# Kernel optimization log

Measured on AMD Instinct MI355X. Metric: run time of the kernel, lower is better.

## Reference

```python
import jax, jax.numpy as jnp
import numpy as np

B, T, E, H = 64, 200, 512, 8
D = E // H          # head size 64
SCALE = E ** -0.5   # NOTE: original scales by EMBED_DIM**-0.5, not head_size**-0.5


def _ln(x, g, b):
    mu = jnp.mean(x, axis=-1, keepdims=True)
    d = x - mu
    v = jnp.mean(d * d, axis=-1, keepdims=True)
    return g * d * jax.lax.rsqrt(v + 1e-5) + b


def _forward(idx, memory, src_mask, pred_mask,
             sa_wq, sa_wk, sa_wv, sa_wo, sa_bo,
             ca_wq, ca_wk, ca_wv, ca_wo, ca_bo,
             f_w1, f_b1, f_w2, f_b2,
             ln1_g, ln1_b, ln2_g, ln2_b, ln3_g, ln3_b):
    causal = jnp.tril(jnp.ones((T, T), dtype=bool))      # [T,T]
    pm = (pred_mask != 0)[:, None, :, None]              # [B,1,T,1]
    sm = (src_mask != 0)[:, None, :, None]               # [B,1,T,1]

    # --- masked multi-head self-attention (query AND key zeroed by pred_mask) ---
    h = _ln(idx, ln1_g, ln1_b)
    q = jnp.where(pm, jnp.einsum('bte,hed->bhtd', h, sa_wq), 0.0)
    k = jnp.where(pm, jnp.einsum('bte,hed->bhtd', h, sa_wk), 0.0)
    v = jnp.einsum('bte,hed->bhtd', h, sa_wv)
    s = jnp.einsum('bhtd,bhsd->bhts', q, k) * SCALE
    s = jnp.where(causal, s, -jnp.inf)
    w = jax.nn.softmax(s, axis=-1)
    o = jnp.einsum('bhts,bhsd->bthd', w, v).reshape(B, T, E)
    idx = o @ sa_wo + sa_bo + idx

    # --- cross-attention: keys from memory (src-masked), VALUES FROM x (per original code) ---
    h = _ln(idx, ln2_g, ln2_b)
    q = jnp.einsum('bte,hed->bhtd', h, ca_wq)
    k = jnp.where(sm, jnp.einsum('bse,hed->bhsd', memory, ca_wk), 0.0)
    v = jnp.einsum('bte,hed->bhtd', h, ca_wv)
    s = jnp.einsum('bhtd,bhsd->bhts', q, k) * SCALE
    s = jnp.where(causal, s, -jnp.inf)   # mask=True in Decoder's ca
    w = jax.nn.softmax(s, axis=-1)
    o = jnp.einsum('bhts,bhsd->bthd', w, v).reshape(B, T, E)
    idx = o @ ca_wo + ca_bo + idx

    # --- feed-forward ---
    h = _ln(idx, ln3_g, ln3_b)
    idx = jax.nn.relu(h @ f_w1 + f_b1) @ f_w2 + f_b2 + idx
    return idx


def setup_inputs() -> dict:
    key = jax.random.key(0)
    ks = jax.random.split(key, 20)
    nrm = lambda k, sh: jax.random.normal(k, sh, jnp.float32) * 0.02
    return {
        'idx': jax.random.normal(ks[0], (B, T, E), jnp.float32),
        'memory': jax.random.normal(ks[1], (B, T, E), jnp.float32),
        'src_mask': jax.random.randint(ks[2], (B, T), 0, 2, jnp.int32),
        'pred_mask': jax.random.randint(ks[3], (B, T), 0, 2, jnp.int32),
        'sa_wq': nrm(ks[4], (H, E, D)), 'sa_wk': nrm(ks[5], (H, E, D)),
        'sa_wv': nrm(ks[6], (H, E, D)),
        'sa_wo': nrm(ks[7], (E, E)), 'sa_bo': jnp.zeros((E,), jnp.float32),
        'ca_wq': nrm(ks[8], (H, E, D)), 'ca_wk': nrm(ks[9], (H, E, D)),
        'ca_wv': nrm(ks[10], (H, E, D)),
        'ca_wo': nrm(ks[11], (E, E)), 'ca_bo': jnp.zeros((E,), jnp.float32),
        'f_w1': nrm(ks[12], (E, 4 * E)), 'f_b1': jnp.zeros((4 * E,), jnp.float32),
        'f_w2': nrm(ks[13], (4 * E, E)), 'f_b2': jnp.zeros((E,), jnp.float32),
        'ln1_g': jnp.ones((E,), jnp.float32), 'ln1_b': jnp.zeros((E,), jnp.float32),
        'ln2_g': jnp.ones((E,), jnp.float32), 'ln2_b': jnp.zeros((E,), jnp.float32),
        'ln3_g': jnp.ones((E,), jnp.float32), 'ln3_b': jnp.zeros((E,), jnp.float32),
    }


def reference(idx, memory, src_mask, pred_mask,
              sa_wq, sa_wk, sa_wv, sa_wo, sa_bo,
              ca_wq, ca_wk, ca_wv, ca_wo, ca_bo,
              f_w1, f_b1, f_w2, f_b2,
              ln1_g, ln1_b, ln2_g, ln2_b, ln3_g, ln3_b):
    return _forward(idx, memory, src_mask, pred_mask,
                    sa_wq, sa_wk, sa_wv, sa_wo, sa_bo,
                    ca_wq, ca_wk, ca_wv, ca_wo, ca_bo,
                    f_w1, f_b1, f_w2, f_b2,
                    ln1_g, ln1_b, ln2_g, ln2_b, ln3_g, ln3_b)
```

## Files before the change

kernel.cpp:

```cpp
#include <hip/hip_runtime.h>
#include <hip/hip_bf16.h>

#define B_ 64
#define T_ 200
#define E_ 512
#define H_ 8
#define D_ 64

static constexpr float SCALE = 0.044194173824159216f;

typedef __attribute__((ext_vector_type(8))) short bf16x8;
typedef __attribute__((ext_vector_type(4))) float f32x4;

static __device__ inline short f2bf(float f) {
    __hip_bfloat16 h = __float2bfloat16(f);
    return *(short*)&h;
}

static __device__ __forceinline__ void gload16(const short* g, short* l) {
    __builtin_amdgcn_global_load_lds(
        (const __attribute__((address_space(1))) void*)g,
        (__attribute__((address_space(3))) void*)l, 16, 0, 0);
}

__global__ void conv_kernel(const float* __restrict__ in,
                            __hip_bfloat16* __restrict__ out, int n) {
    int i = blockIdx.x * blockDim.x + threadIdx.x;
    if (i < n) out[i] = __float2bfloat16(in[i]);
}

template <int MODE>
__global__ void wt_kernel(const float* __restrict__ in,
                          __hip_bfloat16* __restrict__ out, int N, int K) {
    int i = blockIdx.x * blockDim.x + threadIdx.x;
    if (i >= N * K) return;
    int n = i / K, k = i - n * K;
    float v;
    if (MODE == 0) {
        v = in[(size_t)k * N + n];
    } else {
        int h = n >> 6, d = n & 63;
        v = in[((size_t)h * K + k) * 64 + d];
    }
    out[i] = __float2bfloat16(v);
}

__global__ __launch_bounds__(256) void ln_kernel(const float* __restrict__ x,
                                                 const float* __restrict__ g,
                                                 const float* __restrict__ bta,
                                                 __hip_bfloat16* __restrict__ out) {
    __shared__ float red[4];
    int row = blockIdx.x;
    const float* xr = x + (size_t)row * E_;
    int tid = threadIdx.x;
    float v0 = xr[tid], v1 = xr[tid + 256];
    float s = v0 + v1;
    for (int off = 32; off; off >>= 1) s += __shfl_down(s, off, 64);
    if ((tid & 63) == 0) red[tid >> 6] = s;
    __syncthreads();
    float mu = (red[0] + red[1] + red[2] + red[3]) * (1.0f / E_);
    __syncthreads();
    float d0 = v0 - mu, d1 = v1 - mu;
    float sq = d0 * d0 + d1 * d1;
    for (int off = 32; off; off >>= 1) sq += __shfl_down(sq, off, 64);
    if ((tid & 63) == 0) red[tid >> 6] = sq;
    __syncthreads();
    float var = (red[0] + red[1] + red[2] + red[3]) * (1.0f / E_);
    float r = rsqrtf(var + 1e-5f);
    out[(size_t)row * E_ + tid] = __float2bfloat16(g[tid] * d0 * r + bta[tid]);
    out[(size_t)row * E_ + tid + 256] =
        __float2bfloat16(g[tid + 256] * d1 * r + bta[tid + 256]);
}

template <int MSK, int RELU, int OM, int RES, int BIAS>
__global__ __launch_bounds__(256) void mgemm_kernel(
    const short* __restrict__ A, const short* __restrict__ BT,
    const float* __restrict__ bias, const int* __restrict__ rmask,
    const float* __restrict__ resid, void* __restrict__ Cv,
    int M, int N, int K, size_t wstep) {
    __shared__ __align__(16) short As[128 * 32];
    __shared__ __align__(16) short Bs[128 * 32];
    int tid = threadIdx.x;
    int wave = tid >> 6, lane = tid & 63;
    int qq = lane >> 4, l15 = lane & 15;
    int m0 = blockIdx.y * 128, n0 = blockIdx.x * 128;
    int wm = (wave & 1) * 64, wn = (wave >> 1) * 64;

    int srow = lane >> 2;
    int scol = ((lane & 3) ^ (srow & 3)) * 8;
    const short* gA = A + (size_t)(m0 + wave * 32 + srow) * K + scol;
    const short* gB = BT + (size_t)(n0 + wave * 32 + srow) * K + scol;
    short* lA = &As[wave * 1024];
    short* lB = &Bs[wave * 1024];
    size_t rstep = (size_t)16 * K;

    int swz = (qq ^ (l15 & 3)) * 8;

    f32x4 acc[4][4] = {};

    for (int k0 = 0; k0 < K; k0 += 32) {
        gload16(gA + k0, lA);
        gload16(gA + k0 + rstep, lA + 512);
        gload16(gB + k0, lB);
        gload16(gB + k0 + rstep, lB + 512);
        __syncthreads();
        bf16x8 af[4], bfr[4];
        #pragma unroll
        for (int i = 0; i < 4; ++i)
            af[i] = *(bf16x8*)(&As[(wm + i * 16 + l15) * 32 + swz]);
        #pragma unroll
        for (int j = 0; j < 4; ++j)
            bfr[j] = *(bf16x8*)(&Bs[(wn + j * 16 + l15) * 32 + swz]);
        #pragma unroll
        for (int i = 0; i < 4; ++i)
            #pragma unroll
            for (int j = 0; j < 4; ++j)
                acc[i][j] = __builtin_amdgcn_mfma_f32_16x16x32_bf16(
                    af[i], bfr[j], acc[i][j], 0, 0, 0);
        __syncthreads();
    }

    #pragma unroll
    for (int i = 0; i < 4; ++i) {
        #pragma unroll
        for (int r = 0; r < 4; ++r) {
            int row = m0 + wm + i * 16 + qq * 4 + r;
            float mval = 1.0f;
            if (MSK) mval = (rmask[row] != 0) ? 1.0f : 0.0f;
            #pragma unroll
            for (int j = 0; j < 4; ++j) {
                int col = n0 + wn + j * 16 + l15;
                float val = acc[i][j][r];
                if (BIAS) val += bias[col];
                if (MSK == 1) val *= mval;
                if (MSK == 2) { if (col < 1024) val *= mval; }
                if (RELU) val = fmaxf(val, 0.0f);
                if (RES) val += resid[(size_t)row * N + col];
                if (OM == 0) {
                    ((float*)Cv)[(size_t)row * N + col] = val;
                } else if (OM == 1) {
                    int b_ = row / T_, t = row - b_ * T_;
                    int hh = col >> 6, d = col & 63;
                    ((__hip_bfloat16*)Cv)[(((size_t)b_ * H_ + hh) * T_ + t) * D_ + d] =
                        __float2bfloat16(val);
                } else if (OM == 3) {
                    int b_ = row / T_, t = row - b_ * T_;
                    int which = col >> 9, cc = col & 511;
                    int hh = cc >> 6, d = cc & 63;
                    ((__hip_bfloat16*)Cv)[(size_t)which * wstep +
                                          (((size_t)b_ * H_ + hh) * T_ + t) * D_ + d] =
                        __float2bfloat16(val);
                } else {
                    ((__hip_bfloat16*)Cv)[(size_t)row * N + col] =
                        __float2bfloat16(val);
                }
            }
        }
    }
}

#define NQT 13
__global__ __launch_bounds__(256) void fattn_kernel(const short* __restrict__ q,
                                                    const short* __restrict__ k,
                                                    const short* __restrict__ v,
                                                    __hip_bfloat16* __restrict__ o) {
    __shared__ __align__(16) short Kf[NQT * 8 * 16 * 8];
    __shared__ __align__(16) short Vf[4 * 28 * 16 * 8];
    __shared__ __align__(16) short Pb[4 * 512];

    int tid = threadIdx.x;
    int wave = tid >> 6, lane = tid & 63;
    int qq = lane >> 4, l15 = lane & 15;
    int bh = blockIdx.x;
    int b = bh >> 3, h = bh & 7;

    const short* kp = k + (size_t)bh * T_ * D_;
    const short* vp = v + (size_t)bh * T_ * D_;
    const short* qp = q + (size_t)bh * T_ * D_;

    for (int idx = tid; idx < 8 * 208; idx += 256) {
        int g = idx / 208, s = idx - g * 208;
        int kt = s >> 4, l = s & 15;
        bf16x8 val;
        if (s < 200) {
            val = *(const bf16x8*)(kp + (size_t)s * 64 + g * 8);
        } else {
            #pragma unroll
            for (int j = 0; j < 8; ++j) val[j] = 0;
        }
        *(bf16x8*)&Kf[((kt * 8 + g) * 16 + l) * 8] = val;
    }
    for (int idx = tid; idx < 28 * 64; idx += 256) {
        int g = idx >> 6, d = idx & 63;
        int nt = d >> 4, dl = d & 15;
        bf16x8 val;
        if (g < 25) {
            #pragma unroll
            for (int j = 0; j < 8; ++j) val[j] = vp[(g * 8 + j) * 64 + d];
        } else {
            #pragma unroll
            for (int j = 0; j < 8; ++j) val[j] = 0;
        }
        *(bf16x8*)&Vf[((nt * 28 + g) * 16 + dl) * 8] = val;
    }
    __syncthreads();

    short* pb = &Pb[wave * 512];

    for (int qt = wave; qt < NQT; qt += 4) {
        int t0 = qt * 16;
        bf16x8 qf[2];
        #pragma unroll
        for (int ks = 0; ks < 2; ++ks)
            qf[ks] = *(const bf16x8*)(qp + (size_t)(t0 + l15) * 64 + ks * 32 + qq * 8);
        f32x4 sc[NQT];
        #pragma unroll
        for (int kt = 0; kt < NQT; ++kt) {
            f32x4 a = {0.f, 0.f, 0.f, 0.f};
            bf16x8 kf0 = *(const bf16x8*)&Kf[((kt * 8 + qq) * 16 + l15) * 8];
            bf16x8 kf1 = *(const bf16x8*)&Kf[((kt * 8 + 4 + qq) * 16 + l15) * 8];
            a = __builtin_amdgcn_mfma_f32_16x16x32_bf16(qf[0], kf0, a, 0, 0, 0);
            a = __builtin_amdgcn_mfma_f32_16x16x32_bf16(qf[1], kf1, a, 0, 0, 0);
            sc[kt] = a;
        }
        #pragma unroll
        for (int kt = 0; kt < NQT; ++kt) {
            #pragma unroll
            for (int r = 0; r < 4; ++r) {
                int col = kt * 16 + l15;
                int rowg = t0 + qq * 4 + r;
                sc[kt][r] = (col <= rowg) ? sc[kt][r] * SCALE : -1e30f;
            }
        }
        float mx[4], sum[4], inv[4];
        #pragma unroll
        for (int r = 0; r < 4; ++r) {
            float m = -1e30f;
            #pragma unroll
            for (int kt = 0; kt < NQT; ++kt) m = fmaxf(m, sc[kt][r]);
            #pragma unroll
            for (int off = 1; off < 16; off <<= 1)
                m = fmaxf(m, __shfl_xor(m, off, 64));
            mx[r] = m;
        }
        #pragma unroll
        for (int r = 0; r < 4; ++r) sum[r] = 0.f;
        #pragma unroll
        for (int kt = 0; kt < NQT; ++kt) {
            #pragma unroll
            for (int r = 0; r < 4; ++r) {
                float e = __expf(sc[kt][r] - mx[r]);
                sc[kt][r] = e;
                sum[r] += e;
            }
        }
        #pragma unroll
        for (int r = 0; r < 4; ++r) {
            float s = sum[r];
            #pragma unroll
            for (int off = 1; off < 16; off <<= 1) s += __shfl_xor(s, off, 64);
            inv[r] = 1.0f / s;
        }
        f32x4 oa[4] = {};
        #pragma unroll
        for (int c = 0; c < 7; ++c) {
            #pragma unroll
            for (int kt2 = 0; kt2 < 2; ++kt2) {
                int kt = c * 2 + kt2;
                int g = kt2 * 2 + (l15 >> 3);
                int jj = l15 & 7;
                #pragma unroll
                for (int r = 0; r < 4; ++r) {
                    float val = (kt < NQT) ? sc[kt][r] : 0.0f;
                    pb[(g * 16 + qq * 4 + r) * 8 + jj] = f2bf(val);
                }
            }
            bf16x8 pf = *(const bf16x8*)&pb[(qq * 16 + l15) * 8];
            #pragma unroll
            for (int nt = 0; nt < 4; ++nt) {
                bf16x8 vf = *(const bf16x8*)&Vf[((nt * 28 + c * 4 + qq) * 16 + l15) * 8];
                oa[nt] = __builtin_amdgcn_mfma_f32_16x16x32_bf16(pf, vf, oa[nt], 0, 0, 0);
            }
        }
        #pragma unroll
        for (int nt = 0; nt < 4; ++nt) {
            #pragma unroll
            for (int r = 0; r < 4; ++r) {
                int t = t0 + qq * 4 + r;
                if (t < T_) {
                    int d = nt * 16 + l15;
                    o[((size_t)b * T_ + t) * E_ + h * D_ + d] =
                        __float2bfloat16(oa[nt][r] * inv[r]);
                }
            }
        }
    }
}

extern "C" void kernel_launch(void* const* d_in, const int* in_sizes, int n_in,
                              void* d_out, int out_size, void* d_ws, size_t ws_size,
                              hipStream_t stream) {
    const float* idx    = (const float*)d_in[0];
    const float* memory = (const float*)d_in[1];
    const int* src_mask  = (const int*)d_in[2];
    const int* pred_mask = (const int*)d_in[3];
    const float* sa_wq = (const float*)d_in[4];
    const float* sa_wk = (const float*)d_in[5];
    const float* sa_wv = (const float*)d_in[6];
    const float* sa_wo = (const float*)d_in[7];
    const float* sa_bo = (const float*)d_in[8];
    const float* ca_wq = (const float*)d_in[9];
    const float* ca_wk = (const float*)d_in[10];
    const float* ca_wv = (const float*)d_in[11];
    const float* ca_wo = (const float*)d_in[12];
    const float* ca_bo = (const float*)d_in[13];
    const float* f_w1  = (const float*)d_in[14];
    const float* f_b1  = (const float*)d_in[15];
    const float* f_w2  = (const float*)d_in[16];
    const float* f_b2  = (const float*)d_in[17];
    const float* ln1_g = (const float*)d_in[18];
    const float* ln1_b = (const float*)d_in[19];
    const float* ln2_g = (const float*)d_in[20];
    const float* ln2_b = (const float*)d_in[21];
    const float* ln3_g = (const float*)d_in[22];
    const float* ln3_b = (const float*)d_in[23];
    float* out = (float*)d_out;

    const size_t BTE = (size_t)B_ * T_ * E_;
    const size_t EE = (size_t)E_ * E_;

    char* p = (char*)d_ws;
    short* qb = (short*)p;            p += BTE * 2;
    short* kb = (short*)p;            p += BTE * 2;
    short* vb = (short*)p;            p += BTE * 2;
    float* x1 = (float*)p;            p += BTE * 4;
    __hip_bfloat16* h_bf   = (__hip_bfloat16*)p; p += BTE * 2;
    __hip_bfloat16* o_bf   = (__hip_bfloat16*)p; p += BTE * 2;
    __hip_bfloat16* mem_bf = (__hip_bfloat16*)p; p += BTE * 2;
    __hip_bfloat16* w_qkv_s = (__hip_bfloat16*)p; p += 3 * EE * 2;
    __hip_bfloat16* w_o_s   = (__hip_bfloat16*)p; p += EE * 2;
    __hip_bfloat16* w_qv_c  = (__hip_bfloat16*)p; p += 2 * EE * 2;
    __hip_bfloat16* w_k_c   = (__hip_bfloat16*)p; p += EE * 2;
    __hip_bfloat16* w_o_c   = (__hip_bfloat16*)p; p += EE * 2;
    __hip_bfloat16* w1T     = (__hip_bfloat16*)p; p += EE * 4 * 2;
    __hip_bfloat16* w2T     = (__hip_bfloat16*)p; p += EE * 4 * 2;
    short* ff_bf = qb;

    const int M = B_ * T_;
    dim3 blk(256);
    dim3 g512(E_ / 128, M / 128);
    dim3 g1024(8, M / 128);
    dim3 g1536(12, M / 128);
    dim3 g2048(16, M / 128);
    int nw = (int)EE;
    int nw4 = (int)EE * 4;

    wt_kernel<1><<<(nw + 255) / 256, 256, 0, stream>>>(sa_wq, w_qkv_s, E_, E_);
    wt_kernel<1><<<(nw + 255) / 256, 256, 0, stream>>>(sa_wk, w_qkv_s + EE, E_, E_);
    wt_kernel<1><<<(nw + 255) / 256, 256, 0, stream>>>(sa_wv, w_qkv_s + 2 * EE, E_, E_);
    wt_kernel<0><<<(nw + 255) / 256, 256, 0, stream>>>(sa_wo, w_o_s, E_, E_);
    wt_kernel<1><<<(nw + 255) / 256, 256, 0, stream>>>(ca_wq, w_qv_c, E_, E_);
    wt_kernel<1><<<(nw + 255) / 256, 256, 0, stream>>>(ca_wv, w_qv_c + EE, E_, E_);
    wt_kernel<1><<<(nw + 255) / 256, 256, 0, stream>>>(ca_wk, w_k_c, E_, E_);
    wt_kernel<0><<<(nw + 255) / 256, 256, 0, stream>>>(ca_wo, w_o_c, E_, E_);
    wt_kernel<0><<<(nw4 + 255) / 256, 256, 0, stream>>>(f_w1, w1T, 4 * E_, E_);
    wt_kernel<0><<<(nw4 + 255) / 256, 256, 0, stream>>>(f_w2, w2T, E_, 4 * E_);
    conv_kernel<<<((int)BTE + 255) / 256, 256, 0, stream>>>(memory, mem_bf, (int)BTE);

    ln_kernel<<<M, 256, 0, stream>>>(idx, ln1_g, ln1_b, h_bf);
    mgemm_kernel<2,0,3,0,0><<<g1536, blk, 0, stream>>>(
        (const short*)h_bf, (const short*)w_qkv_s, nullptr, pred_mask, nullptr,
        qb, M, 3 * E_, E_, BTE);
    fattn_kernel<<<B_ * H_, 256, 0, stream>>>(qb, kb, vb, o_bf);
    mgemm_kernel<0,0,0,1,1><<<g512, blk, 0, stream>>>(
        (const short*)o_bf, (const short*)w_o_s, sa_bo, nullptr, idx, x1,
        M, E_, E_, 0);

    ln_kernel<<<M, 256, 0, stream>>>(x1, ln2_g, ln2_b, h_bf);
    mgemm_kernel<0,0,3,0,0><<<g1024, blk, 0, stream>>>(
        (const short*)h_bf, (const short*)w_qv_c, nullptr, nullptr, nullptr,
        qb, M, 2 * E_, E_, 2 * BTE);
    mgemm_kernel<1,0,1,0,0><<<g512, blk, 0, stream>>>(
        (const short*)mem_bf, (const short*)w_k_c, nullptr, src_mask, nullptr,
        kb, M, E_, E_, 0);
    fattn_kernel<<<B_ * H_, 256, 0, stream>>>(qb, kb, vb, o_bf);
    mgemm_kernel<0,0,0,1,1><<<g512, blk, 0, stream>>>(
        (const short*)o_bf, (const short*)w_o_c, ca_bo, nullptr, x1, out,
        M, E_, E_, 0);

    ln_kernel<<<M, 256, 0, stream>>>(out, ln3_g, ln3_b, h_bf);
    mgemm_kernel<0,1,2,0,1><<<g2048, blk, 0, stream>>>(
        (const short*)h_bf, (const short*)w1T, f_b1, nullptr, nullptr,
        ff_bf, M, 4 * E_, E_, 0);
    mgemm_kernel<0,0,0,1,1><<<g512, blk, 0, stream>>>(
        (const short*)ff_bf, (const short*)w2T, f_b2, nullptr, out, out,
        M, E_, 4 * E_, 0);
}
```

Measured before the change: 511.6 us.

## Double-buffer GEMM loads, remap blocks across XCDs, tile weight transposes, vectorize conversion

The GEMM kernel now double-buffers its LDS tiles. It issues the next K-slice's global-to-LDS loads before computing the current one and uses a partial vmcnt wait with raw barriers, so load latency overlaps with MFMA work. Workgroup indices are remapped so that consecutive tiles land on the same XCD for better L2 locality, and the LDS swizzle pattern is changed. Separately, the weight transpose kernels use a shared-memory tiled transpose for coalesced reads and writes, and the memory fp32-to-bf16 conversion is vectorized to 4 elements per thread. The trade-off is doubled LDS use per block, which may lower occupancy.

```diff
diff --git a/kernel.cpp b/kernel.cpp
--- a/kernel.cpp
+++ b/kernel.cpp
@@ -10,6 +10,7 @@
 static constexpr float SCALE = 0.044194173824159216f;
 
 typedef __attribute__((ext_vector_type(8))) short bf16x8;
+typedef __attribute__((ext_vector_type(4))) short bf16x4;
 typedef __attribute__((ext_vector_type(4))) float f32x4;
 
 static __device__ inline short f2bf(float f) {
@@ -25,24 +26,41 @@
 
 __global__ void conv_kernel(const float* __restrict__ in,
                             __hip_bfloat16* __restrict__ out, int n) {
-    int i = blockIdx.x * blockDim.x + threadIdx.x;
-    if (i < n) out[i] = __float2bfloat16(in[i]);
+    int i = (blockIdx.x * blockDim.x + threadIdx.x) * 4;
+    if (i < n) {
+        f32x4 v = *(const f32x4*)(in + i);
+        bf16x4 r;
+        #pragma unroll
+        for (int j = 0; j < 4; ++j) r[j] = f2bf(v[j]);
+        *(bf16x4*)((short*)out + i) = r;
+    }
 }
 
 template <int MODE>
-__global__ void wt_kernel(const float* __restrict__ in,
-                          __hip_bfloat16* __restrict__ out, int N, int K) {
-    int i = blockIdx.x * blockDim.x + threadIdx.x;
-    if (i >= N * K) return;
-    int n = i / K, k = i - n * K;
-    float v;
-    if (MODE == 0) {
-        v = in[(size_t)k * N + n];
-    } else {
-        int h = n >> 6, d = n & 63;
-        v = in[((size_t)h * K + k) * 64 + d];
-    }
-    out[i] = __float2bfloat16(v);
+__global__ __launch_bounds__(256) void wt_kernel(const float* __restrict__ in,
+                                                 __hip_bfloat16* __restrict__ out,
+                                                 int N, int K) {
+    __shared__ float tile[64][65];
+    int n0 = blockIdx.x * 64, k0 = blockIdx.y * 64;
+    int tx = threadIdx.x & 63, ty = threadIdx.x >> 6;
+    #pragma unroll
+    for (int i = 0; i < 16; ++i) {
+        int k = k0 + ty + i * 4;
+        float v;
+        if (MODE == 0) {
+            v = in[(size_t)k * N + n0 + tx];
+        } else {
+            int h = n0 >> 6;
+            v = in[((size_t)h * K + k) * 64 + tx];
+        }
+        tile[ty + i * 4][tx] = v;
+    }
+    __syncthreads();
+    #pragma unroll
+    for (int i = 0; i < 16; ++i) {
+        int n = ty + i * 4;
+        out[(size_t)(n0 + n) * K + k0 + tx] = __float2bfloat16(tile[tx][n]);
+    }
 }
 
 __global__ __launch_bounds__(256) void ln_kernel(const float* __restrict__ x,
@@ -78,46 +96,67 @@
     const float* __restrict__ bias, const int* __restrict__ rmask,
     const float* __restrict__ resid, void* __restrict__ Cv,
     int M, int N, int K, size_t wstep) {
-    __shared__ __align__(16) short As[128 * 32];
-    __shared__ __align__(16) short Bs[128 * 32];
+    __shared__ __align__(16) short As[2][128 * 32];
+    __shared__ __align__(16) short Bs[2][128 * 32];
     int tid = threadIdx.x;
     int wave = tid >> 6, lane = tid & 63;
     int qq = lane >> 4, l15 = lane & 15;
-    int m0 = blockIdx.y * 128, n0 = blockIdx.x * 128;
+
+    int nwg = gridDim.x * gridDim.y;
+    int flat = blockIdx.y * gridDim.x + blockIdx.x;
+    int xcd = flat & 7, bix = flat >> 3;
+    int qw = nwg >> 3, rw = nwg & 7;
+    int nf = (xcd < rw ? xcd * (qw + 1) : rw * (qw + 1) + (xcd - rw) * qw) + bix;
+    int by = nf / gridDim.x, bx = nf - by * gridDim.x;
+    int m0 = by * 128, n0 = bx * 128;
     int wm = (wave & 1) * 64, wn = (wave >> 1) * 64;
 
     int srow = lane >> 2;
-    int scol = ((lane & 3) ^ (srow & 3)) * 8;
+    int scol = ((lane & 3) ^ ((srow >> 1) & 3)) * 8;
     const short* gA = A + (size_t)(m0 + wave * 32 + srow) * K + scol;
     const short* gB = BT + (size_t)(n0 + wave * 32 + srow) * K + scol;
-    short* lA = &As[wave * 1024];
-    short* lB = &Bs[wave * 1024];
+    int lofs = wave * 1024;
     size_t rstep = (size_t)16 * K;
 
-    int swz = (qq ^ (l15 & 3)) * 8;
+    int swz = (qq ^ ((l15 >> 1) & 3)) * 8;
 
     f32x4 acc[4][4] = {};
 
-    for (int k0 = 0; k0 < K; k0 += 32) {
-        gload16(gA + k0, lA);
-        gload16(gA + k0 + rstep, lA + 512);
-        gload16(gB + k0, lB);
-        gload16(gB + k0 + rstep, lB + 512);
-        __syncthreads();
+    gload16(gA, &As[0][lofs]);
+    gload16(gA + rstep, &As[0][lofs + 512]);
+    gload16(gB, &Bs[0][lofs]);
+    gload16(gB + rstep, &Bs[0][lofs + 512]);
+
+    int nk = K >> 5;
+    for (int it = 0; it < nk; ++it) {
+        int cur = it & 1;
+        if (it + 1 < nk) {
+            int k1 = (it + 1) << 5;
+            int nxt = cur ^ 1;
+            gload16(gA + k1, &As[nxt][lofs]);
+            gload16(gA + k1 + rstep, &As[nxt][lofs + 512]);
+            gload16(gB + k1, &Bs[nxt][lofs]);
+            gload16(gB + k1 + rstep, &Bs[nxt][lofs + 512]);
+            asm volatile("s_waitcnt vmcnt(4)" ::: "memory");
+        } else {
+            asm volatile("s_waitcnt vmcnt(0)" ::: "memory");
+        }
+        __builtin_amdgcn_s_barrier();
         bf16x8 af[4], bfr[4];
         #pragma unroll
         for (int i = 0; i < 4; ++i)
-            af[i] = *(bf16x8*)(&As[(wm + i * 16 + l15) * 32 + swz]);
+            af[i] = *(bf16x8*)(&As[cur][(wm + i * 16 + l15) * 32 + swz]);
         #pragma unroll
         for (int j = 0; j < 4; ++j)
-            bfr[j] = *(bf16x8*)(&Bs[(wn + j * 16 + l15) * 32 + swz]);
+            bfr[j] = *(bf16x8*)(&Bs[cur][(wn + j * 16 + l15) * 32 + swz]);
         #pragma unroll
         for (int i = 0; i < 4; ++i)
             #pragma unroll
             for (int j = 0; j < 4; ++j)
                 acc[i][j] = __builtin_amdgcn_mfma_f32_16x16x32_bf16(
                     af[i], bfr[j], acc[i][j], 0, 0, 0);
-        __syncthreads();
+        asm volatile("" ::: "memory");
+        __builtin_amdgcn_s_barrier();
     }
 
     #pragma unroll
@@ -352,20 +391,20 @@
     dim3 g1024(8, M / 128);
     dim3 g1536(12, M / 128);
     dim3 g2048(16, M / 128);
-    int nw = (int)EE;
-    int nw4 = (int)EE * 4;
-
-    wt_kernel<1><<<(nw + 255) / 256, 256, 0, stream>>>(sa_wq, w_qkv_s, E_, E_);
-    wt_kernel<1><<<(nw + 255) / 256, 256, 0, stream>>>(sa_wk, w_qkv_s + EE, E_, E_);
-    wt_kernel<1><<<(nw + 255) / 256, 256, 0, stream>>>(sa_wv, w_qkv_s + 2 * EE, E_, E_);
-    wt_kernel<0><<<(nw + 255) / 256, 256, 0, stream>>>(sa_wo, w_o_s, E_, E_);
-    wt_kernel<1><<<(nw + 255) / 256, 256, 0, stream>>>(ca_wq, w_qv_c, E_, E_);
-    wt_kernel<1><<<(nw + 255) / 256, 256, 0, stream>>>(ca_wv, w_qv_c + EE, E_, E_);
-    wt_kernel<1><<<(nw + 255) / 256, 256, 0, stream>>>(ca_wk, w_k_c, E_, E_);
-    wt_kernel<0><<<(nw + 255) / 256, 256, 0, stream>>>(ca_wo, w_o_c, E_, E_);
-    wt_kernel<0><<<(nw4 + 255) / 256, 256, 0, stream>>>(f_w1, w1T, 4 * E_, E_);
-    wt_kernel<0><<<(nw4 + 255) / 256, 256, 0, stream>>>(f_w2, w2T, E_, 4 * E_);
-    conv_kernel<<<((int)BTE + 255) / 256, 256, 0, stream>>>(memory, mem_bf, (int)BTE);
+
+    dim3 t512(8, 8), t_w1(32, 8), t_w2(8, 32);
+    wt_kernel<1><<<t512, blk, 0, stream>>>(sa_wq, w_qkv_s, E_, E_);
+    wt_kernel<1><<<t512, blk, 0, stream>>>(sa_wk, w_qkv_s + EE, E_, E_);
+    wt_kernel<1><<<t512, blk, 0, stream>>>(sa_wv, w_qkv_s + 2 * EE, E_, E_);
+    wt_kernel<0><<<t512, blk, 0, stream>>>(sa_wo, w_o_s, E_, E_);
+    wt_kernel<1><<<t512, blk, 0, stream>>>(ca_wq, w_qv_c, E_, E_);
+    wt_kernel<1><<<t512, blk, 0, stream>>>(ca_wv, w_qv_c + EE, E_, E_);
+    wt_kernel<1><<<t512, blk, 0, stream>>>(ca_wk, w_k_c, E_, E_);
+    wt_kernel<0><<<t512, blk, 0, stream>>>(ca_wo, w_o_c, E_, E_);
+    wt_kernel<0><<<t_w1, blk, 0, stream>>>(f_w1, w1T, 4 * E_, E_);
+    wt_kernel<0><<<t_w2, blk, 0, stream>>>(f_w2, w2T, E_, 4 * E_);
+    conv_kernel<<<((int)(BTE / 4) + 255) / 256, 256, 0, stream>>>(memory, mem_bf,
+                                                                  (int)BTE);
 
     ln_kernel<<<M, 256, 0, stream>>>(idx, ln1_g, ln1_b, h_bf);
     mgemm_kernel<2,0,3,0,0><<<g1536, blk, 0, stream>>>(
```

Result: faster. 458.0 us (-10.5%).
